# Kernel optimization log

Hardware: AMD Instinct MI355X
Metric: run time of the kernel (lower is better)

The kernel has to match this reference:

```python
import jax, jax.numpy as jnp
import numpy as np

B, N, F_DIM = 32, 1024, 128
ALPHA = 0.2        # LeakyReLU negative slope
PAD = -9e15        # pad_sequence padding value in the original
DENSITY = 0.05


def setup_inputs() -> dict:
    key = jax.random.key(0)
    k1, k2, k3 = jax.random.split(key, 3)
    # sparse 0/1 adjacency with self-loops so every node has degree >= 1
    adj = (jax.random.uniform(k1, (B, N, N)) < DENSITY).astype(jnp.float32)
    eye = jnp.eye(N, dtype=jnp.float32)[None, :, :]
    adj = jnp.maximum(adj, eye)
    feats = jax.random.normal(k2, (B, N, F_DIM), dtype=jnp.float32)
    # xavier_uniform with leaky_relu gain on a [2F, 1]
    gain = float(np.sqrt(2.0 / (1.0 + ALPHA ** 2)))
    bound = gain * float(np.sqrt(6.0 / (2 * F_DIM + 1)))
    a = jax.random.uniform(k3, (2 * F_DIM, 1), minval=-bound, maxval=bound,
                           dtype=jnp.float32)
    return {"batch_graphs": adj, "batch_features": feats, "a": a}


def reference(batch_graphs, batch_features, a):
    # e_ij = LeakyReLU([h_i || h_j] @ a) decomposes as (h_i @ a1) + (h_j @ a2)
    s_src = batch_features @ a[:F_DIM, 0]   # [B, N] contribution of node i
    s_dst = batch_features @ a[F_DIM:, 0]   # [B, N] contribution of neighbor j
    e = s_src[:, :, None] + s_dst[:, None, :]            # [B, N, N]
    e = jnp.where(e >= 0, e, ALPHA * e)                   # LeakyReLU
    mask = batch_graphs == 1
    e = jnp.where(mask, e, PAD)                           # pad non-edges like pad_sequence
    att = jax.nn.softmax(e, axis=-1)                      # segmented softmax over neighbors
    att = jnp.where(mask, att, 0.0)                       # scatter back only real edges
    return att
```

## Files before the change

### kernel.cpp

```cpp
#include <hip/hip_runtime.h>
#include <hip/hip_bf16.h>
#include <stdint.h>

#define B_DIM 32
#define N_DIM 1024
#define F_DIM 128
#define ALPHA 0.2f
#define NROWS (B_DIM * N_DIM)
#define TAIL_ROWS 192
#define MAIN_ROWS (NROWS - TAIL_ROWS)
#define SCORE_BYTES ((size_t)(3 * NROWS) * sizeof(float))

typedef float          vf4 __attribute__((ext_vector_type(4)));
typedef unsigned short vh4 __attribute__((ext_vector_type(4)));
typedef unsigned int   vu4 __attribute__((ext_vector_type(4)));

__device__ __forceinline__ unsigned short f32_to_bf16_bits(float f) {
    union { __hip_bfloat16 h; unsigned short u; } cvt;
    cvt.h = __float2bfloat16(f);
    return cvt.u;
}

__device__ __forceinline__ bool probe_is_f32(const void* adj) {
    return *(const uint32_t*)adj == 0x3F800000u;
}

template <bool F32>
__device__ __forceinline__ float* score_base(void* out) {
    const size_t out_bytes = (size_t)NROWS * N_DIM * (F32 ? 4 : 2);
    return (float*)((char*)out + out_bytes - SCORE_BYTES);
}

__device__ __forceinline__ float leaky(float t) { return fmaxf(t, ALPHA * t); }

template <bool F32>
__device__ __forceinline__ void scores_body(
    const void* __restrict__ feats_v, const void* __restrict__ a_v, void* out)
{
    float* base  = score_base<F32>(out);
    float* s_src = base;
    float* s_dst = base + NROWS;

    const int wid  = threadIdx.x >> 6;
    const int lane = threadIdx.x & 63;
    const int row  = blockIdx.x * 4 + wid;
    const int f0   = lane * 2;

    float x0, x1, a10, a11, a20, a21;
    if (F32) {
        const float* fp = (const float*)feats_v + (size_t)row * F_DIM + f0;
        const float* ap = (const float*)a_v;
        x0 = fp[0]; x1 = fp[1];
        a10 = ap[f0];         a11 = ap[f0 + 1];
        a20 = ap[F_DIM + f0]; a21 = ap[F_DIM + f0 + 1];
    } else {
        const __hip_bfloat16* fp = (const __hip_bfloat16*)feats_v + (size_t)row * F_DIM + f0;
        const __hip_bfloat16* ap = (const __hip_bfloat16*)a_v;
        x0  = __bfloat162float(fp[0]);           x1  = __bfloat162float(fp[1]);
        a10 = __bfloat162float(ap[f0]);          a11 = __bfloat162float(ap[f0 + 1]);
        a20 = __bfloat162float(ap[F_DIM + f0]);  a21 = __bfloat162float(ap[F_DIM + f0 + 1]);
    }

    float v1 = x0 * a10 + x1 * a11;
    float v2 = x0 * a20 + x1 * a21;
    #pragma unroll
    for (int off = 32; off > 0; off >>= 1) {
        v1 += __shfl_down(v1, off, 64);
        v2 += __shfl_down(v2, off, 64);
    }
    if (lane == 0) { s_src[row] = v1; s_dst[row] = v2; }
}

__global__ __launch_bounds__(256) void scores_kernel(
    const void* __restrict__ adj, const void* __restrict__ feats,
    const void* __restrict__ a, void* out)
{
    if (probe_is_f32(adj)) scores_body<true>(feats, a, out);
    else                   scores_body<false>(feats, a, out);
}

template <bool F32>
__device__ __forceinline__ void sum_body(const void* __restrict__ adj_v, void* out_v)
{
    const int wid  = threadIdx.x >> 6;
    const int lane = threadIdx.x & 63;
    const int row  = blockIdx.x * 4 + wid;
    const int b    = row >> 10;

    float* base = score_base<F32>(out_v);
    const float  ssrc = base[row];
    const float* sdst = base + NROWS + (size_t)b * N_DIM;

    float lsum = 0.0f;
    #pragma unroll
    for (int c = 0; c < 4; ++c) {
        const int idx = c * 64 + lane;
        const vf4 sd = ((const vf4*)sdst)[idx];
        const float sdk[4] = {sd.x, sd.y, sd.z, sd.w};
        bool v[4];
        if (F32) {
            const vu4 av = ((const vu4*)((const float*)adj_v + (size_t)row * N_DIM))[idx];
            v[0] = av.x != 0u; v[1] = av.y != 0u; v[2] = av.z != 0u; v[3] = av.w != 0u;
        } else {
            const vh4 av = ((const vh4*)((const __hip_bfloat16*)adj_v + (size_t)row * N_DIM))[idx];
            v[0] = av.x != 0; v[1] = av.y != 0; v[2] = av.z != 0; v[3] = av.w != 0;
        }
        #pragma unroll
        for (int k = 0; k < 4; ++k)
            lsum += v[k] ? __expf(leaky(ssrc + sdk[k])) : 0.0f;
    }

    #pragma unroll
    for (int off = 1; off < 64; off <<= 1)
        lsum += __shfl_xor(lsum, off, 64);

    if (lane == 0) (base + 2 * NROWS)[row] = 1.0f / lsum;
}

__global__ __launch_bounds__(256) void sum_kernel(
    const void* __restrict__ adj, void* out)
{
    if (probe_is_f32(adj)) sum_body<true>(adj, out);
    else                   sum_body<false>(adj, out);
}

template <bool F32>
__device__ __forceinline__ void map_body(const void* __restrict__ adj_v, void* out_v)
{
    const int row = blockIdx.x;
    const int b   = row >> 10;
    const int tid = threadIdx.x;

    const float* base = score_base<F32>(out_v);
    const float  ssrc = base[row];
    const float  iv   = (base + 2 * NROWS)[row];
    const vf4    sd   = ((const vf4*)(base + NROWS + (size_t)b * N_DIM))[tid];
    const float  sdk[4] = {sd.x, sd.y, sd.z, sd.w};

    bool v[4];
    if (F32) {
        const vu4 av = ((const vu4*)((const float*)adj_v + (size_t)row * N_DIM))[tid];
        v[0] = av.x != 0u; v[1] = av.y != 0u; v[2] = av.z != 0u; v[3] = av.w != 0u;
    } else {
        const vh4 av = ((const vh4*)((const __hip_bfloat16*)adj_v + (size_t)row * N_DIM))[tid];
        v[0] = av.x != 0; v[1] = av.y != 0; v[2] = av.z != 0; v[3] = av.w != 0;
    }

    float q[4];
    #pragma unroll
    for (int k = 0; k < 4; ++k)
        q[k] = v[k] ? __expf(leaky(ssrc + sdk[k])) * iv : 0.0f;

    if (F32) {
        vf4 o; o.x = q[0]; o.y = q[1]; o.z = q[2]; o.w = q[3];
        ((vf4*)((float*)out_v + (size_t)row * N_DIM))[tid] = o;
    } else {
        vh4 o;
        o.x = f32_to_bf16_bits(q[0]); o.y = f32_to_bf16_bits(q[1]);
        o.z = f32_to_bf16_bits(q[2]); o.w = f32_to_bf16_bits(q[3]);
        ((vh4*)((__hip_bfloat16*)out_v + (size_t)row * N_DIM))[tid] = o;
    }
}

__global__ __launch_bounds__(256) void map_kernel(
    const void* __restrict__ adj, void* out)
{
    if (probe_is_f32(adj)) map_body<true>(adj, out);
    else                   map_body<false>(adj, out);
}

template <bool F32>
__device__ __forceinline__ void tail_body(
    const void* __restrict__ adj_v, const void* __restrict__ feats_v,
    const void* __restrict__ a_v, void* __restrict__ out_v)
{
    __shared__ float sdst_sh[N_DIM];

    const int tid  = threadIdx.x;
    const int wid  = tid >> 6;
    const int lane = tid & 63;
    const int b    = B_DIM - 1;
    const int row  = MAIN_ROWS + blockIdx.x * 4 + wid;

    #pragma unroll
    for (int k = 0; k < 4; ++k) {
        const int j = tid * 4 + k;
        float acc = 0.0f;
        if (F32) {
            const vf4* fp = (const vf4*)((const float*)feats_v + ((size_t)b * N_DIM + j) * F_DIM);
            const vf4* ap = (const vf4*)((const float*)a_v + F_DIM);
            #pragma unroll 8
            for (int f = 0; f < F_DIM / 4; ++f) {
                const vf4 x = fp[f], w = ap[f];
                acc += x.x * w.x + x.y * w.y + x.z * w.z + x.w * w.w;
            }
        } else {
            const __hip_bfloat16* fp = (const __hip_bfloat16*)feats_v + ((size_t)b * N_DIM + j) * F_DIM;
            const __hip_bfloat16* ap = (const __hip_bfloat16*)a_v + F_DIM;
            #pragma unroll 8
            for (int f = 0; f < F_DIM; ++f)
                acc += __bfloat162float(fp[f]) * __bfloat162float(ap[f]);
        }
        sdst_sh[j] = acc;
    }

    float ssrc;
    {
        const int f0 = lane * 2;
        float x0, x1, a0, a1;
        if (F32) {
            const float* fp = (const float*)feats_v + (size_t)row * F_DIM + f0;
            const float* ap = (const float*)a_v;
            x0 = fp[0]; x1 = fp[1]; a0 = ap[f0]; a1 = ap[f0 + 1];
        } else {
            const __hip_bfloat16* fp = (const __hip_bfloat16*)feats_v + (size_t)row * F_DIM + f0;
            const __hip_bfloat16* ap = (const __hip_bfloat16*)a_v;
            x0 = __bfloat162float(fp[0]); x1 = __bfloat162float(fp[1]);
            a0 = __bfloat162float(ap[f0]); a1 = __bfloat162float(ap[f0 + 1]);
        }
        float s = x0 * a0 + x1 * a1;
        #pragma unroll
        for (int off = 32; off > 0; off >>= 1)
            s += __shfl_down(s, off, 64);
        ssrc = __shfl(s, 0, 64);
    }
    __syncthreads();

    float p[16], lsum = 0.0f;
    #pragma unroll
    for (int c = 0; c < 4; ++c) {
        const int idx = c * 64 + lane;
        const vf4 sd = ((const vf4*)sdst_sh)[idx];
        const float sdk[4] = {sd.x, sd.y, sd.z, sd.w};
        bool v[4];
        if (F32) {
            const vu4 av = ((const vu4*)((const float*)adj_v + (size_t)row * N_DIM))[idx];
            v[0] = av.x != 0u; v[1] = av.y != 0u; v[2] = av.z != 0u; v[3] = av.w != 0u;
        } else {
            const vh4 av = ((const vh4*)((const __hip_bfloat16*)adj_v + (size_t)row * N_DIM))[idx];
            v[0] = av.x != 0; v[1] = av.y != 0; v[2] = av.z != 0; v[3] = av.w != 0;
        }
        #pragma unroll
        for (int k = 0; k < 4; ++k) {
            const float q = v[k] ? __expf(leaky(ssrc + sdk[k])) : 0.0f;
            p[c*4+k] = q;
            lsum += q;
        }
    }
    #pragma unroll
    for (int off = 1; off < 64; off <<= 1)
        lsum += __shfl_xor(lsum, off, 64);
    const float inv = 1.0f / lsum;

    #pragma unroll
    for (int c = 0; c < 4; ++c) {
        const int idx = c * 64 + lane;
        if (F32) {
            vf4 o;
            o.x = p[c*4+0] * inv; o.y = p[c*4+1] * inv;
            o.z = p[c*4+2] * inv; o.w = p[c*4+3] * inv;
            ((vf4*)((float*)out_v + (size_t)row * N_DIM))[idx] = o;
        } else {
            vh4 o;
            o.x = f32_to_bf16_bits(p[c*4+0] * inv);
            o.y = f32_to_bf16_bits(p[c*4+1] * inv);
            o.z = f32_to_bf16_bits(p[c*4+2] * inv);
            o.w = f32_to_bf16_bits(p[c*4+3] * inv);
            ((vh4*)((__hip_bfloat16*)out_v + (size_t)row * N_DIM))[idx] = o;
        }
    }
}

__global__ __launch_bounds__(256) void tail_kernel(
    const void* __restrict__ adj, const void* __restrict__ feats,
    const void* __restrict__ a, void* __restrict__ out)
{
    if (probe_is_f32(adj)) tail_body<true>(adj, feats, a, out);
    else                   tail_body<false>(adj, feats, a, out);
}

extern "C" void kernel_launch(void* const* d_in, const int* in_sizes, int n_in,
                              void* d_out, int out_size, void* d_ws, size_t ws_size,
                              hipStream_t stream) {
    const void* adj   = d_in[0];
    const void* feats = d_in[1];
    const void* a     = d_in[2];
    (void)d_ws; (void)ws_size;

    scores_kernel<<<NROWS / 4,     256, 0, stream>>>(adj, feats, a, d_out);
    sum_kernel   <<<MAIN_ROWS / 4, 256, 0, stream>>>(adj, d_out);
    map_kernel   <<<MAIN_ROWS,     256, 0, stream>>>(adj, d_out);
    tail_kernel  <<<TAIL_ROWS / 4, 256, 0, stream>>>(adj, feats, a, d_out);
}
```

Baseline: 276.7 us.

## Compress adjacency to bitmask in reduce pass and reuse it in write pass

The reduce kernel now records each row's adjacency as 16 ballot bitmasks in a scratch area at the end of the output buffer. The write kernel reads these bits instead of re-reading the full adjacency row, which removes a second full read of the dense adjacency. The scratch region grows to hold the masks, so the tail region processed by the separate tail kernel is enlarged to 2240 rows, and the tail kernel now derives the batch index from the row. The risk is a larger serialized tail kernel and extra scratch writes.

```diff
diff --git a/kernel.cpp b/kernel.cpp
--- a/kernel.cpp
+++ b/kernel.cpp
@@ -7,13 +7,14 @@
 #define F_DIM 128
 #define ALPHA 0.2f
 #define NROWS (B_DIM * N_DIM)
-#define TAIL_ROWS 192
+#define TAIL_ROWS 2240
 #define MAIN_ROWS (NROWS - TAIL_ROWS)
-#define SCORE_BYTES ((size_t)(3 * NROWS) * sizeof(float))
+#define SCRATCH_BYTES ((size_t)NROWS * (3 * 4 + 16 * 8))
 
 typedef float          vf4 __attribute__((ext_vector_type(4)));
 typedef unsigned short vh4 __attribute__((ext_vector_type(4)));
 typedef unsigned int   vu4 __attribute__((ext_vector_type(4)));
+typedef unsigned long long u64;
 
 __device__ __forceinline__ unsigned short f32_to_bf16_bits(float f) {
     union { __hip_bfloat16 h; unsigned short u; } cvt;
@@ -28,7 +29,10 @@
 template <bool F32>
 __device__ __forceinline__ float* score_base(void* out) {
     const size_t out_bytes = (size_t)NROWS * N_DIM * (F32 ? 4 : 2);
-    return (float*)((char*)out + out_bytes - SCORE_BYTES);
+    return (float*)((char*)out + out_bytes - SCRATCH_BYTES);
+}
+__device__ __forceinline__ u64* mask_base(float* base) {
+    return (u64*)(base + 3 * NROWS);
 }
 
 __device__ __forceinline__ float leaky(float t) { return fmaxf(t, ALPHA * t); }
@@ -80,7 +84,7 @@
 }
 
 template <bool F32>
-__device__ __forceinline__ void sum_body(const void* __restrict__ adj_v, void* out_v)
+__device__ __forceinline__ void reduce_body(const void* __restrict__ adj_v, void* out_v)
 {
     const int wid  = threadIdx.x >> 6;
     const int lane = threadIdx.x & 63;
@@ -90,6 +94,7 @@
     float* base = score_base<F32>(out_v);
     const float  ssrc = base[row];
     const float* sdst = base + NROWS + (size_t)b * N_DIM;
+    u64* mrow = mask_base(base) + (size_t)row * 16;
 
     float lsum = 0.0f;
     #pragma unroll
@@ -106,50 +111,48 @@
             v[0] = av.x != 0; v[1] = av.y != 0; v[2] = av.z != 0; v[3] = av.w != 0;
         }
         #pragma unroll
-        for (int k = 0; k < 4; ++k)
+        for (int k = 0; k < 4; ++k) {
             lsum += v[k] ? __expf(leaky(ssrc + sdk[k])) : 0.0f;
+            const u64 blt = __ballot(v[k]);
+            if (lane == 0) mrow[c * 4 + k] = blt;
+        }
     }
 
     #pragma unroll
     for (int off = 1; off < 64; off <<= 1)
         lsum += __shfl_xor(lsum, off, 64);
-
     if (lane == 0) (base + 2 * NROWS)[row] = 1.0f / lsum;
 }
 
-__global__ __launch_bounds__(256) void sum_kernel(
+__global__ __launch_bounds__(256) void reduce_kernel(
     const void* __restrict__ adj, void* out)
 {
-    if (probe_is_f32(adj)) sum_body<true>(adj, out);
-    else                   sum_body<false>(adj, out);
-}
-
-template <bool F32>
-__device__ __forceinline__ void map_body(const void* __restrict__ adj_v, void* out_v)
+    if (probe_is_f32(adj)) reduce_body<true>(adj, out);
+    else                   reduce_body<false>(adj, out);
+}
+
+template <bool F32>
+__device__ __forceinline__ void write_body(void* __restrict__ out_v)
 {
     const int row = blockIdx.x;
     const int b   = row >> 10;
     const int tid = threadIdx.x;
-
-    const float* base = score_base<F32>(out_v);
-    const float  ssrc = base[row];
-    const float  iv   = (base + 2 * NROWS)[row];
-    const vf4    sd   = ((const vf4*)(base + NROWS + (size_t)b * N_DIM))[tid];
-    const float  sdk[4] = {sd.x, sd.y, sd.z, sd.w};
-
-    bool v[4];
-    if (F32) {
-        const vu4 av = ((const vu4*)((const float*)adj_v + (size_t)row * N_DIM))[tid];
-        v[0] = av.x != 0u; v[1] = av.y != 0u; v[2] = av.z != 0u; v[3] = av.w != 0u;
-    } else {
-        const vh4 av = ((const vh4*)((const __hip_bfloat16*)adj_v + (size_t)row * N_DIM))[tid];
-        v[0] = av.x != 0; v[1] = av.y != 0; v[2] = av.z != 0; v[3] = av.w != 0;
-    }
+    const int c   = tid >> 6;
+    const int L   = tid & 63;
+
+    float* base = score_base<F32>(out_v);
+    const float ssrc = base[row];
+    const float iv   = (base + 2 * NROWS)[row];
+    const vf4   sd   = ((const vf4*)(base + NROWS + (size_t)b * N_DIM))[tid];
+    const float sdk[4] = {sd.x, sd.y, sd.z, sd.w};
+    const u64*  mw   = mask_base(base) + (size_t)row * 16 + c * 4;
 
     float q[4];
     #pragma unroll
-    for (int k = 0; k < 4; ++k)
-        q[k] = v[k] ? __expf(leaky(ssrc + sdk[k])) * iv : 0.0f;
+    for (int k = 0; k < 4; ++k) {
+        const bool v = (mw[k] >> L) & 1;
+        q[k] = v ? __expf(leaky(ssrc + sdk[k])) * iv : 0.0f;
+    }
 
     if (F32) {
         vf4 o; o.x = q[0]; o.y = q[1]; o.z = q[2]; o.w = q[3];
@@ -162,11 +165,11 @@
     }
 }
 
-__global__ __launch_bounds__(256) void map_kernel(
+__global__ __launch_bounds__(256) void write_kernel(
     const void* __restrict__ adj, void* out)
 {
-    if (probe_is_f32(adj)) map_body<true>(adj, out);
-    else                   map_body<false>(adj, out);
+    if (probe_is_f32(adj)) write_body<true>(out);
+    else                   write_body<false>(out);
 }
 
 template <bool F32>
@@ -179,8 +182,9 @@
     const int tid  = threadIdx.x;
     const int wid  = tid >> 6;
     const int lane = tid & 63;
-    const int b    = B_DIM - 1;
-    const int row  = MAIN_ROWS + blockIdx.x * 4 + wid;
+    const int row0 = MAIN_ROWS + blockIdx.x * 4;
+    const int b    = row0 >> 10;
+    const int row  = row0 + wid;
 
     #pragma unroll
     for (int k = 0; k < 4; ++k) {
@@ -287,8 +291,8 @@
     const void* a     = d_in[2];
     (void)d_ws; (void)ws_size;
 
-    scores_kernel<<<NROWS / 4,     256, 0, stream>>>(adj, feats, a, d_out);
-    sum_kernel   <<<MAIN_ROWS / 4, 256, 0, stream>>>(adj, d_out);
-    map_kernel   <<<MAIN_ROWS,     256, 0, stream>>>(adj, d_out);
-    tail_kernel  <<<TAIL_ROWS / 4, 256, 0, stream>>>(adj, feats, a, d_out);
-}
+    scores_kernel<<<NROWS / 4,      256, 0, stream>>>(adj, feats, a, d_out);
+    reduce_kernel<<<MAIN_ROWS / 4,  256, 0, stream>>>(adj, d_out);
+    write_kernel <<<MAIN_ROWS,      256, 0, stream>>>(adj, d_out);
+    tail_kernel  <<<TAIL_ROWS / 4,  256, 0, stream>>>(adj, feats, a, d_out);
+}
```

Result: slower. 294.8 us (+6.5%).
